# Performance work log

Measured on AMD Instinct MI355X. Metric: run time of the kernel, lower is better.

The kernel has to match this reference:

```python
import jax, jax.numpy as jnp
import numpy as np

N_HEADS = 4
D_K = 64
SCALE = D_K ** (-0.5)


def setup_inputs() -> dict:
    key = jax.random.key(0)
    k1, k2, k3, k4, k5 = jax.random.split(key, 5)
    B, C, H, W = 16, 256, 32, 32
    x = jax.random.normal(k1, (B, C, H, W), dtype=jnp.float32)
    # Linear weights stored as (in, out) for x @ W convention
    w_qkv = jax.random.normal(k2, (C, N_HEADS * D_K * 3), dtype=jnp.float32) * (C ** -0.5)
    b_qkv = jax.random.normal(k3, (N_HEADS * D_K * 3,), dtype=jnp.float32) * 0.02
    w_out = jax.random.normal(k4, (N_HEADS * D_K, C), dtype=jnp.float32) * ((N_HEADS * D_K) ** -0.5)
    b_out = jax.random.normal(k5, (C,), dtype=jnp.float32) * 0.02
    return {"x": x, "w_qkv": w_qkv, "b_qkv": b_qkv, "w_out": w_out, "b_out": b_out}


def reference(x, w_qkv, b_qkv, w_out, b_out):
    # NOTE: the original torch module defines GroupNorm but never applies it
    # in forward; we faithfully reproduce the forward as written.
    B, C, H, W = x.shape
    S = H * W
    xs = x.reshape(B, C, S).transpose(0, 2, 1)            # [B, S, C]
    qkv = (xs @ w_qkv + b_qkv).reshape(B, S, N_HEADS, 3 * D_K)
    q, k, v = jnp.split(qkv, 3, axis=-1)                   # each [B, S, H, d_k]
    attn = jnp.einsum('bihd,bjhd->bijh', q, k) * SCALE     # [B, S, S, H]
    attn = jax.nn.softmax(attn, axis=2)                    # softmax over j (keys)
    res = jnp.einsum('bijh,bjhd->bihd', attn, v)           # [B, S, H, d_k]
    res = res.reshape(B, S, N_HEADS * D_K)
    res = res @ w_out + b_out + xs                         # residual add
    return res.transpose(0, 2, 1).reshape(B, C, H, W)
```

## Files before the change

### kernel.cpp

```cpp
#include <hip/hip_runtime.h>
#include <hip/hip_bf16.h>

typedef __attribute__((ext_vector_type(8))) short short8;
typedef __attribute__((ext_vector_type(4))) short short4v;
typedef __attribute__((ext_vector_type(4))) float floatx4;
typedef unsigned short u16;

#define SCL_LOG2E 0.1803368801111204f

__device__ inline u16 f2b(float f) {
  __hip_bfloat16 h = __float2bfloat16(f);
  union { __hip_bfloat16 h; u16 u; } cv; cv.h = h; return cv.u;
}

__global__ __launch_bounds__(256) void tr64_f32_bf16(const float* __restrict__ in,
                                                     u16* __restrict__ out,
                                                     int R, int Cc) {
  __shared__ u16 tile[64][72];
  int bz = blockIdx.z;
  const float* inb = in + (size_t)bz * R * Cc;
  u16* outb = out + (size_t)bz * R * Cc;
  int c0 = blockIdx.x * 64, r0 = blockIdx.y * 64;
  int tx = threadIdx.x, ty = threadIdx.y;
#pragma unroll
  for (int i = 0; i < 4; i++) {
    int r = ty + 16 * i;
    float4 v = *(const float4*)&inb[(size_t)(r0 + r) * Cc + c0 + tx * 4];
    tile[tx * 4 + 0][r] = f2b(v.x);
    tile[tx * 4 + 1][r] = f2b(v.y);
    tile[tx * 4 + 2][r] = f2b(v.z);
    tile[tx * 4 + 3][r] = f2b(v.w);
  }
  __syncthreads();
#pragma unroll
  for (int i = 0; i < 4; i++) {
    int cc = ty + 16 * i;
    ushort4 o = *(ushort4*)&tile[cc][tx * 4];
    *(ushort4*)&outb[(size_t)(c0 + cc) * R + r0 + tx * 4] = o;
  }
}

__global__ __launch_bounds__(256) void qkv_gemm(const u16* __restrict__ xs,
                                                const float* __restrict__ wq,
                                                const float* __restrict__ bias,
                                                u16* __restrict__ Qo,
                                                u16* __restrict__ Ko,
                                                u16* __restrict__ Vto) {
  __shared__ u16 As[128 * 32];
  __shared__ u16 Bs[128 * 40];
  const int tid = threadIdx.x, wave = tid >> 6, lane = tid & 63;
  const int l15 = lane & 15, quad = lane >> 4;
  const int wm = (wave >> 1) * 64, wn = (wave & 1) * 64;
  const int m0 = blockIdx.x * 128, n0 = blockIdx.y * 128;
  const int bb = m0 >> 10, s0 = m0 & 1023;
  const int srow = wave * 32 + (lane >> 2), scol = (lane & 3) * 8;
  const int cl = tid >> 3, u = tid & 7;

  floatx4 acc[4][4] = {};

  for (int kt = 0; kt < 256; kt += 32) {
#pragma unroll
    for (int i = 0; i < 2; i++) {
      int r = srow + i * 16;
      *(short8*)&As[r * 32 + scol] =
          *(const short8*)&xs[((size_t)(bb * 1024 + s0 + r)) * 256 + kt + scol];
    }
    const float* wr = wq + (size_t)(kt + cl) * 768 + n0;
#pragma unroll
    for (int j = 0; j < 4; j++) {
      int e = u * 4 + 32 * j;
      float4 vb = *(const float4*)&wr[e];
      Bs[(e + 0) * 40 + cl] = f2b(vb.x);
      Bs[(e + 1) * 40 + cl] = f2b(vb.y);
      Bs[(e + 2) * 40 + cl] = f2b(vb.z);
      Bs[(e + 3) * 40 + cl] = f2b(vb.w);
    }
    __syncthreads();
    short8 af[4], bfr[4];
#pragma unroll
    for (int mi = 0; mi < 4; mi++)
      af[mi] = *(short8*)&As[(wm + mi * 16 + l15) * 32 + quad * 8];
#pragma unroll
    for (int ni = 0; ni < 4; ni++)
      bfr[ni] = *(short8*)&Bs[(wn + ni * 16 + l15) * 40 + quad * 8];
#pragma unroll
    for (int mi = 0; mi < 4; mi++)
#pragma unroll
      for (int ni = 0; ni < 4; ni++)
        acc[mi][ni] = __builtin_amdgcn_mfma_f32_16x16x32_bf16(af[mi], bfr[ni],
                                                              acc[mi][ni], 0, 0, 0);
    __syncthreads();
  }

#pragma unroll
  for (int ni = 0; ni < 4; ni++) {
    int n = n0 + wn + ni * 16 + l15;
    float bvv = bias[n];
    int h = n / 192;
    int rem = n - h * 192;
#pragma unroll
    for (int mi = 0; mi < 4; mi++) {
      int gm = m0 + wm + mi * 16 + quad * 4;
      int s = gm & 1023;
      if (rem < 128) {
        u16* dst;
        float scl;
        if (rem < 64) { dst = Qo; scl = SCL_LOG2E; } else { dst = Ko; scl = 1.0f; }
        int d = rem & 63;
#pragma unroll
        for (int r = 0; r < 4; r++)
          dst[((size_t)(bb * 4 + h) * 1024 + s + r) * 64 + d] =
              f2b((acc[mi][ni][r] + bvv) * scl);
      } else {
        int d = rem - 128;
        ushort4 pk;
        pk.x = f2b(acc[mi][ni][0] + bvv);
        pk.y = f2b(acc[mi][ni][1] + bvv);
        pk.z = f2b(acc[mi][ni][2] + bvv);
        pk.w = f2b(acc[mi][ni][3] + bvv);
        *(ushort4*)&Vto[((size_t)(bb * 4 + h) * 64 + d) * 1024 + s] = pk;
      }
    }
  }
}

__global__ __launch_bounds__(256, 2) void attn_kern(const u16* __restrict__ Q,
                                                    const u16* __restrict__ K,
                                                    const u16* __restrict__ Vt,
                                                    u16* __restrict__ O) {
  __shared__ u16 kv[3 * 2 * 64 * 72];
  const int bh = blockIdx.x;
  const u16* Qp = Q + (size_t)bh * 64 * 1024;
  const u16* Kp = K + (size_t)bh * 64 * 1024;
  const u16* Vp = Vt + (size_t)bh * 64 * 1024;
  u16* Op = O + (size_t)bh * 64 * 1024;
  const int q0 = blockIdx.y * 128;
  const int tid = threadIdx.x, wave = tid >> 6, lane = tid & 63;
  const int l15 = lane & 15, quad = lane >> 4;

  short8 qa[2][2];
#pragma unroll
  for (int qi = 0; qi < 2; qi++)
#pragma unroll
    for (int kh = 0; kh < 2; kh++)
      qa[qi][kh] = *(const short8*)&Qp[(size_t)(q0 + wave * 32 + qi * 16 + l15) * 64 +
                                       kh * 32 + quad * 8];

  const int srow = tid >> 2;
  const int sc = (tid & 3) * 16;
  const size_t kRow = (size_t)srow * 64 + sc;
  const size_t vRow = (size_t)srow * 1024 + sc;

  short8 t0k0 = *(const short8*)&Kp[kRow];
  short8 t0k1 = *(const short8*)&Kp[kRow + 8];
  short8 t0v0 = *(const short8*)&Vp[vRow];
  short8 t0v1 = *(const short8*)&Vp[vRow + 8];
  short8 t1k0 = *(const short8*)&Kp[kRow + 4096];
  short8 t1k1 = *(const short8*)&Kp[kRow + 4096 + 8];
  short8 t1v0 = *(const short8*)&Vp[vRow + 64];
  short8 t1v1 = *(const short8*)&Vp[vRow + 64 + 8];
  short8 r1k0 = *(const short8*)&Kp[kRow + 8192];
  short8 r1k1 = *(const short8*)&Kp[kRow + 8192 + 8];
  short8 r1v0 = *(const short8*)&Vp[vRow + 128];
  short8 r1v1 = *(const short8*)&Vp[vRow + 128 + 8];
  *(short8*)&kv[srow * 72 + sc] = t0k0;
  *(short8*)&kv[srow * 72 + sc + 8] = t0k1;
  *(short8*)&kv[4608 + srow * 72 + sc] = t0v0;
  *(short8*)&kv[4608 + srow * 72 + sc + 8] = t0v1;
  *(short8*)&kv[9216 + srow * 72 + sc] = t1k0;
  *(short8*)&kv[9216 + srow * 72 + sc + 8] = t1k1;
  *(short8*)&kv[9216 + 4608 + srow * 72 + sc] = t1v0;
  *(short8*)&kv[9216 + 4608 + srow * 72 + sc + 8] = t1v1;
  __syncthreads();

  float lsum[2] = {0.f, 0.f};
  floatx4 acc[2][4] = {};

  int cur = 0;
  int wr = 2;
  for (int t = 0; t < 16; t++) {
    const u16* Ksb = kv + cur * 9216;
    const u16* Vsb = Ksb + 4608;

    short8 r2k0, r2k1, r2v0, r2v1;
    if (t < 13) {
      size_t ko = kRow + (size_t)(t + 3) * 4096;
      size_t vo = vRow + (size_t)(t + 3) * 64;
      r2k0 = *(const short8*)&Kp[ko];
      r2k1 = *(const short8*)&Kp[ko + 8];
      r2v0 = *(const short8*)&Vp[vo];
      r2v1 = *(const short8*)&Vp[vo + 8];
    }

    short8 kb[4][2];
#pragma unroll
    for (int mj = 0; mj < 4; mj++)
#pragma unroll
      for (int kh = 0; kh < 2; kh++)
        kb[mj][kh] = *(const short8*)&Ksb[(mj * 16 + l15) * 72 + kh * 32 + quad * 8];

    floatx4 sf[2][4];
#pragma unroll
    for (int qi = 0; qi < 2; qi++)
#pragma unroll
      for (int mj = 0; mj < 4; mj++) {
        floatx4 z = {};
        z = __builtin_amdgcn_mfma_f32_16x16x32_bf16(kb[mj][0], qa[qi][0], z, 0, 0, 0);
        sf[qi][mj] =
            __builtin_amdgcn_mfma_f32_16x16x32_bf16(kb[mj][1], qa[qi][1], z, 0, 0, 0);
      }

    short4v pb[2][4];
#pragma unroll
    for (int qi = 0; qi < 2; qi++)
#pragma unroll
      for (int mj = 0; mj < 4; mj++) {
        float p0 = exp2f(sf[qi][mj][0]), p1 = exp2f(sf[qi][mj][1]);
        float p2 = exp2f(sf[qi][mj][2]), p3 = exp2f(sf[qi][mj][3]);
        lsum[qi] += (p0 + p1) + (p2 + p3);
        short4v pk;
        pk[0] = (short)f2b(p0); pk[1] = (short)f2b(p1);
        pk[2] = (short)f2b(p2); pk[3] = (short)f2b(p3);
        pb[qi][mj] = pk;
      }

#pragma unroll
    for (int c = 0; c < 4; c++)
#pragma unroll
      for (int md = 0; md < 4; md++) {
        short4v va = *(const short4v*)&Vsb[(md * 16 + l15) * 72 + c * 16 + quad * 4];
#pragma unroll
        for (int qi = 0; qi < 2; qi++)
          acc[qi][md] =
              __builtin_amdgcn_mfma_f32_16x16x16bf16_1k(va, pb[qi][c], acc[qi][md],
                                                        0, 0, 0);
      }

    if (t < 14) {
      u16* dst = kv + wr * 9216;
      *(short8*)&dst[srow * 72 + sc] = r1k0;
      *(short8*)&dst[srow * 72 + sc + 8] = r1k1;
      *(short8*)&dst[4608 + srow * 72 + sc] = r1v0;
      *(short8*)&dst[4608 + srow * 72 + sc + 8] = r1v1;
    }
    r1k0 = r2k0; r1k1 = r2k1; r1v0 = r2v0; r1v1 = r2v1;
    cur = (cur == 2) ? 0 : cur + 1;
    wr = (wr == 2) ? 0 : wr + 1;
    __syncthreads();
  }

  float inv[2];
#pragma unroll
  for (int qi = 0; qi < 2; qi++) {
    lsum[qi] += __shfl_xor(lsum[qi], 16, 64);
    lsum[qi] += __shfl_xor(lsum[qi], 32, 64);
    inv[qi] = 1.f / lsum[qi];
  }

  u16* Ot = kv;
#pragma unroll
  for (int qi = 0; qi < 2; qi++)
#pragma unroll
    for (int md = 0; md < 4; md++) {
      uint2 pk;
      u16 a0 = f2b(acc[qi][md][0] * inv[qi]), a1 = f2b(acc[qi][md][1] * inv[qi]);
      u16 a2 = f2b(acc[qi][md][2] * inv[qi]), a3 = f2b(acc[qi][md][3] * inv[qi]);
      pk.x = (unsigned)a0 | ((unsigned)a1 << 16);
      pk.y = (unsigned)a2 | ((unsigned)a3 << 16);
      *(uint2*)&Ot[(wave * 32 + qi * 16 + l15) * 72 + md * 16 + quad * 4] = pk;
    }
  __syncthreads();
#pragma unroll
  for (int rr = 0; rr < 4; rr++) {
    int row = wave * 32 + (lane >> 3) + 8 * rr;
    int col = (lane & 7) * 8;
    short8 v = *(const short8*)&Ot[row * 72 + col];
    *(short8*)&Op[(size_t)(q0 + row) * 64 + col] = v;
  }
}

__global__ __launch_bounds__(256) void out_gemm(const u16* __restrict__ Oin,
                                                const float* __restrict__ wo,
                                                const float* __restrict__ bias,
                                                const float* __restrict__ x,
                                                float* __restrict__ out) {
  __shared__ u16 As[64 * 32];
  __shared__ u16 Bs[128 * 40];
  const int tid = threadIdx.x, wave = tid >> 6, lane = tid & 63;
  const int l15 = lane & 15, quad = lane >> 4;
  const int wm = (wave >> 1) * 32, wn = (wave & 1) * 64;
  const int m0 = blockIdx.x * 64, n0 = blockIdx.y * 128;
  const int bb = m0 >> 10, s0 = m0 & 1023;
  const int ar = tid >> 2, ach = (tid & 3) * 8;
  const int cl = tid >> 3, u = tid & 7;

  floatx4 acc[2][4] = {};

  for (int kt = 0; kt < 256; kt += 32) {
    int h = kt >> 6, d0 = kt & 63;
    *(short8*)&As[ar * 32 + ach] =
        *(const short8*)&Oin[((size_t)(bb * 4 + h) * 1024 + s0 + ar) * 64 + d0 + ach];
    const float* wr = wo + (size_t)(kt + cl) * 256 + n0;
#pragma unroll
    for (int j = 0; j < 4; j++) {
      int e = u * 4 + 32 * j;
      float4 vb = *(const float4*)&wr[e];
      Bs[(e + 0) * 40 + cl] = f2b(vb.x);
      Bs[(e + 1) * 40 + cl] = f2b(vb.y);
      Bs[(e + 2) * 40 + cl] = f2b(vb.z);
      Bs[(e + 3) * 40 + cl] = f2b(vb.w);
    }
    __syncthreads();
    short8 af[2], bfr[4];
#pragma unroll
    for (int mi = 0; mi < 2; mi++)
      af[mi] = *(short8*)&As[(wm + mi * 16 + l15) * 32 + quad * 8];
#pragma unroll
    for (int ni = 0; ni < 4; ni++)
      bfr[ni] = *(short8*)&Bs[(wn + ni * 16 + l15) * 40 + quad * 8];
#pragma unroll
    for (int mi = 0; mi < 2; mi++)
#pragma unroll
      for (int ni = 0; ni < 4; ni++)
        acc[mi][ni] = __builtin_amdgcn_mfma_f32_16x16x32_bf16(af[mi], bfr[ni],
                                                              acc[mi][ni], 0, 0, 0);
    __syncthreads();
  }

#pragma unroll
  for (int ni = 0; ni < 4; ni++) {
    int c = n0 + wn + ni * 16 + l15;
    float bvv = bias[c];
#pragma unroll
    for (int mi = 0; mi < 2; mi++) {
      int gm = m0 + wm + mi * 16 + quad * 4;
      int s = gm & 1023;
      size_t idx = ((size_t)bb * 256 + c) * 1024 + s;
      float4 xr = *(const float4*)&x[idx];
      float4 o;
      o.x = acc[mi][ni][0] + bvv + xr.x;
      o.y = acc[mi][ni][1] + bvv + xr.y;
      o.z = acc[mi][ni][2] + bvv + xr.z;
      o.w = acc[mi][ni][3] + bvv + xr.w;
      *(float4*)&out[idx] = o;
    }
  }
}

extern "C" void kernel_launch(void* const* d_in, const int* in_sizes, int n_in,
                              void* d_out, int out_size, void* d_ws, size_t ws_size,
                              hipStream_t stream) {
  const float* x     = (const float*)d_in[0];
  const float* w_qkv = (const float*)d_in[1];
  const float* b_qkv = (const float*)d_in[2];
  const float* w_out = (const float*)d_in[3];
  const float* b_out = (const float*)d_in[4];
  float* out = (float*)d_out;
  char* ws = (char*)d_ws;

  u16* xs  = (u16*)(ws);
  u16* Qb  = (u16*)(ws + 8388608);
  u16* Kb  = (u16*)(ws + 16777216);
  u16* Vtb = (u16*)(ws + 25165824);
  u16* Ob  = xs;

  tr64_f32_bf16<<<dim3(16, 4, 16), dim3(16, 16), 0, stream>>>(x, xs, 256, 1024);
  qkv_gemm<<<dim3(128, 6), 256, 0, stream>>>(xs, w_qkv, b_qkv, Qb, Kb, Vtb);
  attn_kern<<<dim3(64, 8), 256, 0, stream>>>(Qb, Kb, Vtb, Ob);
  out_gemm<<<dim3(256, 2), 256, 0, stream>>>(Ob, w_out, b_out, x, out);
}
```

Baseline: 141.9 us.

## Pre-transpose weights to bf16, fuse x conversion into QKV GEMM, double-buffer loads

The separate x transpose/convert kernel is replaced by a small weight-prep kernel that transposes both weight matrices to bf16 once per call. The QKV GEMM now reads fp32 x directly, converting and transposing it into double-buffered shared memory, and loads weight fragments straight from global memory into registers with one-step prefetch. out_gemm likewise drops its shared-memory B tile and prefetches the next A and B tiles. The aim is to remove the 8 MB bf16 x round trip and the per-block weight conversion, at the cost of uncoalesced-looking global weight fragment loads and added register pressure.

```diff
diff --git a/kernel.cpp b/kernel.cpp
--- a/kernel.cpp
+++ b/kernel.cpp
@@ -13,19 +13,21 @@
   union { __hip_bfloat16 h; u16 u; } cv; cv.h = h; return cv.u;
 }
 
-__global__ __launch_bounds__(256) void tr64_f32_bf16(const float* __restrict__ in,
-                                                     u16* __restrict__ out,
-                                                     int R, int Cc) {
+__global__ __launch_bounds__(256) void wprep(const float* __restrict__ w1,
+                                             const float* __restrict__ w2,
+                                             u16* __restrict__ o1,
+                                             u16* __restrict__ o2) {
   __shared__ u16 tile[64][72];
-  int bz = blockIdx.z;
-  const float* inb = in + (size_t)bz * R * Cc;
-  u16* outb = out + (size_t)bz * R * Cc;
-  int c0 = blockIdx.x * 64, r0 = blockIdx.y * 64;
+  const int R = 256;
+  const float* in; u16* out; int Cc, cb;
+  if (blockIdx.x < 12) { in = w1; out = o1; Cc = 768; cb = blockIdx.x; }
+  else                 { in = w2; out = o2; Cc = 256; cb = blockIdx.x - 12; }
+  int c0 = cb * 64, r0 = blockIdx.y * 64;
   int tx = threadIdx.x, ty = threadIdx.y;
 #pragma unroll
   for (int i = 0; i < 4; i++) {
     int r = ty + 16 * i;
-    float4 v = *(const float4*)&inb[(size_t)(r0 + r) * Cc + c0 + tx * 4];
+    float4 v = *(const float4*)&in[(size_t)(r0 + r) * Cc + c0 + tx * 4];
     tile[tx * 4 + 0][r] = f2b(v.x);
     tile[tx * 4 + 1][r] = f2b(v.y);
     tile[tx * 4 + 2][r] = f2b(v.z);
@@ -36,53 +38,70 @@
   for (int i = 0; i < 4; i++) {
     int cc = ty + 16 * i;
     ushort4 o = *(ushort4*)&tile[cc][tx * 4];
-    *(ushort4*)&outb[(size_t)(c0 + cc) * R + r0 + tx * 4] = o;
-  }
-}
-
-__global__ __launch_bounds__(256) void qkv_gemm(const u16* __restrict__ xs,
-                                                const float* __restrict__ wq,
-                                                const float* __restrict__ bias,
-                                                u16* __restrict__ Qo,
-                                                u16* __restrict__ Ko,
-                                                u16* __restrict__ Vto) {
-  __shared__ u16 As[128 * 32];
-  __shared__ u16 Bs[128 * 40];
+    *(ushort4*)&out[(size_t)(c0 + cc) * R + r0 + tx * 4] = o;
+  }
+}
+
+__global__ __launch_bounds__(256, 3) void qkv_gemm(const float* __restrict__ x,
+                                                   const u16* __restrict__ wT,
+                                                   const float* __restrict__ bias,
+                                                   u16* __restrict__ Qo,
+                                                   u16* __restrict__ Ko,
+                                                   u16* __restrict__ Vto) {
+  __shared__ u16 As[2][128 * 36];
   const int tid = threadIdx.x, wave = tid >> 6, lane = tid & 63;
   const int l15 = lane & 15, quad = lane >> 4;
   const int wm = (wave >> 1) * 64, wn = (wave & 1) * 64;
   const int m0 = blockIdx.x * 128, n0 = blockIdx.y * 128;
   const int bb = m0 >> 10, s0 = m0 & 1023;
-  const int srow = wave * 32 + (lane >> 2), scol = (lane & 3) * 8;
-  const int cl = tid >> 3, u = tid & 7;
+  const int cr = tid >> 3, uu = tid & 7;
+
+  const float* xrow = x + ((size_t)bb * 256 + cr) * 1024 + s0 + uu * 4;
+  const u16* wrow[4];
+#pragma unroll
+  for (int ni = 0; ni < 4; ni++)
+    wrow[ni] = wT + (size_t)(n0 + wn + ni * 16 + l15) * 256 + quad * 8;
 
   floatx4 acc[4][4] = {};
-
-  for (int kt = 0; kt < 256; kt += 32) {
-#pragma unroll
-    for (int i = 0; i < 2; i++) {
-      int r = srow + i * 16;
-      *(short8*)&As[r * 32 + scol] =
-          *(const short8*)&xs[((size_t)(bb * 1024 + s0 + r)) * 256 + kt + scol];
-    }
-    const float* wr = wq + (size_t)(kt + cl) * 768 + n0;
-#pragma unroll
-    for (int j = 0; j < 4; j++) {
-      int e = u * 4 + 32 * j;
-      float4 vb = *(const float4*)&wr[e];
-      Bs[(e + 0) * 40 + cl] = f2b(vb.x);
-      Bs[(e + 1) * 40 + cl] = f2b(vb.y);
-      Bs[(e + 2) * 40 + cl] = f2b(vb.z);
-      Bs[(e + 3) * 40 + cl] = f2b(vb.w);
+  float4 LA[4];
+  short8 bfr[4], nbf[4];
+
+#pragma unroll
+  for (int r = 0; r < 4; r++) LA[r] = *(const float4*)&xrow[r * 32];
+#pragma unroll
+  for (int ni = 0; ni < 4; ni++) bfr[ni] = *(const short8*)&wrow[ni][0];
+#pragma unroll
+  for (int r = 0; r < 4; r++) {
+    int s = uu * 4 + r * 32;
+    As[0][(s + 0) * 36 + cr] = f2b(LA[r].x);
+    As[0][(s + 1) * 36 + cr] = f2b(LA[r].y);
+    As[0][(s + 2) * 36 + cr] = f2b(LA[r].z);
+    As[0][(s + 3) * 36 + cr] = f2b(LA[r].w);
+  }
+
+  int cur = 0;
+  for (int kt8 = 0; kt8 < 8; kt8++) {
+    const int kt = kt8 * 32;
+    if (kt8 < 7) {
+#pragma unroll
+      for (int r = 0; r < 4; r++)
+        LA[r] = *(const float4*)&xrow[(size_t)(kt + 32) * 1024 + r * 32];
+#pragma unroll
+      for (int ni = 0; ni < 4; ni++)
+        nbf[ni] = *(const short8*)&wrow[ni][kt + 32];
     }
     __syncthreads();
-    short8 af[4], bfr[4];
-#pragma unroll
-    for (int mi = 0; mi < 4; mi++)
-      af[mi] = *(short8*)&As[(wm + mi * 16 + l15) * 32 + quad * 8];
-#pragma unroll
-    for (int ni = 0; ni < 4; ni++)
-      bfr[ni] = *(short8*)&Bs[(wn + ni * 16 + l15) * 40 + quad * 8];
+    short8 af[4];
+#pragma unroll
+    for (int mi = 0; mi < 4; mi++) {
+      const u16* p = &As[cur][(wm + mi * 16 + l15) * 36 + quad * 8];
+      ushort4 lo = *(const ushort4*)p;
+      ushort4 hi = *(const ushort4*)(p + 4);
+      short8 v;
+      v[0] = lo.x; v[1] = lo.y; v[2] = lo.z; v[3] = lo.w;
+      v[4] = hi.x; v[5] = hi.y; v[6] = hi.z; v[7] = hi.w;
+      af[mi] = v;
+    }
 #pragma unroll
     for (int mi = 0; mi < 4; mi++)
 #pragma unroll
@@ -90,6 +109,20 @@
         acc[mi][ni] = __builtin_amdgcn_mfma_f32_16x16x32_bf16(af[mi], bfr[ni],
                                                               acc[mi][ni], 0, 0, 0);
     __syncthreads();
+    if (kt8 < 7) {
+      u16* d = &As[cur ^ 1][0];
+#pragma unroll
+      for (int r = 0; r < 4; r++) {
+        int s = uu * 4 + r * 32;
+        d[(s + 0) * 36 + cr] = f2b(LA[r].x);
+        d[(s + 1) * 36 + cr] = f2b(LA[r].y);
+        d[(s + 2) * 36 + cr] = f2b(LA[r].z);
+        d[(s + 3) * 36 + cr] = f2b(LA[r].w);
+      }
+#pragma unroll
+      for (int ni = 0; ni < 4; ni++) bfr[ni] = nbf[ni];
+      cur ^= 1;
+    }
   }
 
 #pragma unroll
@@ -280,44 +313,44 @@
 }
 
 __global__ __launch_bounds__(256) void out_gemm(const u16* __restrict__ Oin,
-                                                const float* __restrict__ wo,
+                                                const u16* __restrict__ wT,
                                                 const float* __restrict__ bias,
                                                 const float* __restrict__ x,
                                                 float* __restrict__ out) {
   __shared__ u16 As[64 * 32];
-  __shared__ u16 Bs[128 * 40];
   const int tid = threadIdx.x, wave = tid >> 6, lane = tid & 63;
   const int l15 = lane & 15, quad = lane >> 4;
   const int wm = (wave >> 1) * 32, wn = (wave & 1) * 64;
   const int m0 = blockIdx.x * 64, n0 = blockIdx.y * 128;
   const int bb = m0 >> 10, s0 = m0 & 1023;
   const int ar = tid >> 2, ach = (tid & 3) * 8;
-  const int cl = tid >> 3, u = tid & 7;
+
+  const u16* wrow[4];
+#pragma unroll
+  for (int ni = 0; ni < 4; ni++)
+    wrow[ni] = wT + (size_t)(n0 + wn + ni * 16 + l15) * 256 + quad * 8;
 
   floatx4 acc[2][4] = {};
-
-  for (int kt = 0; kt < 256; kt += 32) {
-    int h = kt >> 6, d0 = kt & 63;
-    *(short8*)&As[ar * 32 + ach] =
-        *(const short8*)&Oin[((size_t)(bb * 4 + h) * 1024 + s0 + ar) * 64 + d0 + ach];
-    const float* wr = wo + (size_t)(kt + cl) * 256 + n0;
-#pragma unroll
-    for (int j = 0; j < 4; j++) {
-      int e = u * 4 + 32 * j;
-      float4 vb = *(const float4*)&wr[e];
-      Bs[(e + 0) * 40 + cl] = f2b(vb.x);
-      Bs[(e + 1) * 40 + cl] = f2b(vb.y);
-      Bs[(e + 2) * 40 + cl] = f2b(vb.z);
-      Bs[(e + 3) * 40 + cl] = f2b(vb.w);
+  short8 LA, bfr[4], nbf[4];
+
+  LA = *(const short8*)&Oin[((size_t)(bb * 4) * 1024 + s0 + ar) * 64 + ach];
+#pragma unroll
+  for (int ni = 0; ni < 4; ni++) bfr[ni] = *(const short8*)&wrow[ni][0];
+  *(short8*)&As[ar * 32 + ach] = LA;
+
+  for (int kt8 = 0; kt8 < 8; kt8++) {
+    const int kt = kt8 * 32;
+    if (kt8 < 7) {
+      int kn = kt + 32, h = kn >> 6, d0 = kn & 63;
+      LA = *(const short8*)&Oin[((size_t)(bb * 4 + h) * 1024 + s0 + ar) * 64 + d0 + ach];
+#pragma unroll
+      for (int ni = 0; ni < 4; ni++) nbf[ni] = *(const short8*)&wrow[ni][kn];
     }
     __syncthreads();
-    short8 af[2], bfr[4];
+    short8 af[2];
 #pragma unroll
     for (int mi = 0; mi < 2; mi++)
       af[mi] = *(short8*)&As[(wm + mi * 16 + l15) * 32 + quad * 8];
-#pragma unroll
-    for (int ni = 0; ni < 4; ni++)
-      bfr[ni] = *(short8*)&Bs[(wn + ni * 16 + l15) * 40 + quad * 8];
 #pragma unroll
     for (int mi = 0; mi < 2; mi++)
 #pragma unroll
@@ -325,6 +358,11 @@
         acc[mi][ni] = __builtin_amdgcn_mfma_f32_16x16x32_bf16(af[mi], bfr[ni],
                                                               acc[mi][ni], 0, 0, 0);
     __syncthreads();
+    if (kt8 < 7) {
+      *(short8*)&As[ar * 32 + ach] = LA;
+#pragma unroll
+      for (int ni = 0; ni < 4; ni++) bfr[ni] = nbf[ni];
+    }
   }
 
 #pragma unroll
@@ -358,14 +396,15 @@
   float* out = (float*)d_out;
   char* ws = (char*)d_ws;
 
-  u16* xs  = (u16*)(ws);
-  u16* Qb  = (u16*)(ws + 8388608);
-  u16* Kb  = (u16*)(ws + 16777216);
-  u16* Vtb = (u16*)(ws + 25165824);
-  u16* Ob  = xs;
-
-  tr64_f32_bf16<<<dim3(16, 4, 16), dim3(16, 16), 0, stream>>>(x, xs, 256, 1024);
-  qkv_gemm<<<dim3(128, 6), 256, 0, stream>>>(xs, w_qkv, b_qkv, Qb, Kb, Vtb);
+  u16* wT1 = (u16*)(ws);
+  u16* wT2 = (u16*)(ws + 0x80000);
+  u16* Qb  = (u16*)(ws + 0x100000);
+  u16* Kb  = (u16*)(ws + 0x900000);
+  u16* Vtb = (u16*)(ws + 0x1100000);
+  u16* Ob  = (u16*)(ws + 0x1900000);
+
+  wprep<<<dim3(16, 4), dim3(16, 16), 0, stream>>>(w_qkv, w_out, wT1, wT2);
+  qkv_gemm<<<dim3(128, 6), 256, 0, stream>>>(x, wT1, b_qkv, Qb, Kb, Vtb);
   attn_kern<<<dim3(64, 8), 256, 0, stream>>>(Qb, Kb, Vtb, Ob);
-  out_gemm<<<dim3(256, 2), 256, 0, stream>>>(Ob, w_out, b_out, x, out);
-}
+  out_gemm<<<dim3(256, 2), 256, 0, stream>>>(Ob, wT2, b_out, x, out);
+}
```

Result: no change. 140.0 us (median of 2 runs) (-1.4%).
